# Performance work log

Measured on AMD Instinct MI355X. Metric: run time of the kernel, lower is better.

The kernel has to match this reference:

```python
import jax, jax.numpy as jnp
import numpy as np

DT = 0.01
NJ = 7
GRAV = 9.81
Q_LOWER = jnp.array([-2.9671, -1.8326, -2.9671, -3.1416, -2.9671, -0.0873, -2.9671], jnp.float32)
Q_UPPER = jnp.array([ 2.9671,  1.8326,  2.9671,  0.0,     2.9671,  3.8223,  2.9671], jnp.float32)


def _skew(v):
    z = jnp.zeros((), v.dtype)
    return jnp.stack([jnp.stack([z, -v[2], v[1]]),
                      jnp.stack([v[2], z, -v[0]]),
                      jnp.stack([-v[1], v[0], z])])


def _mot_X(E, r):
    # 6x6 spatial motion transform [[E,0],[-E*skew(r),E]]
    zero = jnp.zeros_like(E)
    top = jnp.concatenate([E, zero], axis=1)
    bot = jnp.concatenate([-E @ _skew(r), E], axis=1)
    return jnp.concatenate([top, bot], axis=0)


def _crm(v):
    # spatial motion cross-product matrix for v=[w;v0]
    Sw, Sv = _skew(v[:3]), _skew(v[3:])
    zero = jnp.zeros_like(Sw)
    top = jnp.concatenate([Sw, zero], axis=1)
    bot = jnp.concatenate([Sv, Sw], axis=1)
    return jnp.concatenate([top, bot], axis=0)


def _step_single(x, u, axes, R_tree, p_tree, I_sp):
    dt_ = x.dtype
    q = jnp.clip(x[:NJ], Q_LOWER.astype(dt_), Q_UPPER.astype(dt_))
    qd = x[NJ:]
    # forward kinematics: per-joint 6x6 child<-parent transforms and motion subspaces
    Xups, Ss = [], []
    eye3 = jnp.eye(3, dtype=dt_)
    for i in range(NJ):
        a = axes[i]
        c, s = jnp.cos(q[i]), jnp.sin(q[i])
        R = c * eye3 + s * _skew(a) + (1.0 - c) * jnp.outer(a, a)  # rodrigues
        Xj = _mot_X(R.T, jnp.zeros(3, dt_))
        Xt = _mot_X(R_tree[i], p_tree[i])
        Xups.append(Xj @ Xt)
        Ss.append(jnp.concatenate([a, jnp.zeros(3, dt_)]))
    # RNEA bias force h (qdd=0, gravity, zero base velocity, identity base pose)
    v_prev = jnp.zeros(6, dt_)
    a_prev = jnp.array([0.0, 0.0, 0.0, 0.0, 0.0, GRAV], dt_)  # a_base = -g trick
    fs = []
    for i in range(NJ):
        vJ = Ss[i] * qd[i]
        v = Xups[i] @ v_prev + vJ
        acc = Xups[i] @ a_prev + _crm(v) @ vJ
        Iv = I_sp[i] @ v
        f = I_sp[i] @ acc - _crm(v).T @ Iv  # crf(v) = -crm(v)^T
        fs.append(f)
        v_prev, a_prev = v, acc
    h = [None] * NJ
    for i in range(NJ - 1, -1, -1):
        h[i] = Ss[i] @ fs[i]
        if i > 0:
            fs[i - 1] = fs[i - 1] + Xups[i].T @ fs[i]
    h = jnp.stack(h)
    # CRBA mass matrix (serial chain, parent(i)=i-1)
    Ic = [I_sp[i] for i in range(NJ)]
    M = jnp.zeros((NJ, NJ), dt_)
    for i in range(NJ - 1, -1, -1):
        if i > 0:
            Ic[i - 1] = Ic[i - 1] + Xups[i].T @ Ic[i] @ Xups[i]
        F = Ic[i] @ Ss[i]
        M = M.at[i, i].set(Ss[i] @ F)
        for j in range(i - 1, -1, -1):
            F = Xups[j + 1].T @ F
            mij = Ss[j] @ F
            M = M.at[i, j].set(mij).at[j, i].set(mij)
    M = M + 1e-8 * jnp.eye(NJ, dtype=dt_)
    qdd = jnp.linalg.solve(M, (u - h)[:, None])[:, 0]
    qd_new = qd + DT * qdd
    q_new = q + DT * qd_new
    return jnp.concatenate([q_new, qd_new])


def setup_inputs() -> dict:
    B = 65536
    key = jax.random.key(0)
    k1, k2 = jax.random.split(key)
    x = jax.random.normal(k1, (B, 14), jnp.float32)
    u = jax.random.normal(k2, (B, 7), jnp.float32)
    rng = np.random.default_rng(0)
    # unit joint axes
    axes = rng.normal(size=(NJ, 3))
    axes = axes / np.linalg.norm(axes, axis=1, keepdims=True)
    # orthonormal fixed parent->child rotations (det +1)
    R_tree = np.empty((NJ, 3, 3))
    for i in range(NJ):
        Q, _ = np.linalg.qr(rng.normal(size=(3, 3)))
        if np.linalg.det(Q) < 0:
            Q[:, 0] = -Q[:, 0]
        R_tree[i] = Q
    p_tree = 0.2 * rng.normal(size=(NJ, 3))
    # SPD 6x6 spatial inertias: [[Ibar, m*Cx],[m*Cx^T, m*I3]]
    I_sp = np.empty((NJ, 6, 6))
    for i in range(NJ):
        m = float(rng.uniform(1.0, 5.0))
        c = 0.05 * rng.normal(size=3)
        Cx = np.array([[0, -c[2], c[1]], [c[2], 0, -c[0]], [-c[1], c[0], 0]])
        A = 0.1 * rng.normal(size=(3, 3))
        Ic_ = A @ A.T + 0.05 * np.eye(3)
        Ibar = Ic_ + m * Cx @ Cx.T
        I_sp[i] = np.block([[Ibar, m * Cx], [m * Cx.T, m * np.eye(3)]])
    return {
        "x": x, "u": u,
        "axes": jnp.asarray(axes, jnp.float32),
        "R_tree": jnp.asarray(R_tree, jnp.float32),
        "p_tree": jnp.asarray(p_tree, jnp.float32),
        "I_sp": jnp.asarray(I_sp, jnp.float32),
    }


def reference(x, u, axes, R_tree, p_tree, I_sp):
    return jax.vmap(_step_single, in_axes=(0, 0, None, None, None, None))(
        x, u, axes, R_tree, p_tree, I_sp)
```

## Files before the change

kernel.cpp:

```cpp
#include <hip/hip_runtime.h>
#include <math.h>

#define NJ 7
#define DTF 0.01f
#define GRAVF 9.81f
#define MIX(i,j) ((i)*((i)+1)/2 + (j))
#define MPAD 29

__device__ __forceinline__ void cross3(const float* a, const float* b, float* o){
    o[0] = a[1]*b[2] - a[2]*b[1];
    o[1] = a[2]*b[0] - a[0]*b[2];
    o[2] = a[0]*b[1] - a[1]*b[0];
}
__device__ __forceinline__ void mv3(const float* E, const float* x, float* y){
    y[0] = E[0]*x[0] + E[1]*x[1] + E[2]*x[2];
    y[1] = E[3]*x[0] + E[4]*x[1] + E[5]*x[2];
    y[2] = E[6]*x[0] + E[7]*x[1] + E[8]*x[2];
}
__device__ __forceinline__ void mtv3(const float* E, const float* x, float* y){
    y[0] = E[0]*x[0] + E[3]*x[1] + E[6]*x[2];
    y[1] = E[1]*x[0] + E[4]*x[1] + E[7]*x[2];
    y[2] = E[2]*x[0] + E[5]*x[1] + E[8]*x[2];
}
__device__ __forceinline__ void mm3(const float* A, const float* B, float* o){
#pragma unroll
    for (int r = 0; r < 3; r++){
#pragma unroll
        for (int c = 0; c < 3; c++){
            o[r*3+c] = A[r*3]*B[c] + A[r*3+1]*B[3+c] + A[r*3+2]*B[6+c];
        }
    }
}
__device__ __forceinline__ void congr(const float* E, const float* X, float* o){
    float t[9];
#pragma unroll
    for (int r = 0; r < 3; r++){
#pragma unroll
        for (int c = 0; c < 3; c++){
            t[r*3+c] = E[r]*X[c] + E[3+r]*X[3+c] + E[6+r]*X[6+c];
        }
    }
    mm3(t, E, o);
}
__device__ __forceinline__ void makeE(const float* a, float s, float c,
                                      const float* Rt, float* Eo){
    float omc = 1.0f - c;
    float RT[9];
    RT[0] = c + omc*a[0]*a[0];       RT[1] =  s*a[2] + omc*a[0]*a[1]; RT[2] = -s*a[1] + omc*a[0]*a[2];
    RT[3] = -s*a[2] + omc*a[1]*a[0]; RT[4] = c + omc*a[1]*a[1];       RT[5] =  s*a[0] + omc*a[1]*a[2];
    RT[6] =  s*a[1] + omc*a[2]*a[0]; RT[7] = -s*a[0] + omc*a[2]*a[1]; RT[8] = c + omc*a[2]*a[2];
    mm3(RT, Rt, Eo);
}

__global__ __launch_bounds__(128)
void panda_step(const float* __restrict__ x, const float* __restrict__ u,
                const float* __restrict__ g_ax, const float* __restrict__ g_Rt,
                const float* __restrict__ g_pt, const float* __restrict__ g_I,
                float* __restrict__ out, int B)
{
    __shared__ float s_ax[NJ*3], s_Rt[NJ*9], s_pt[NJ*3], s_A[NJ*9], s_h[NJ*3], s_m[NJ];
    __shared__ float s_M[64*MPAD];
    if (threadIdx.x < NJ){
        int i = threadIdx.x;
#pragma unroll
        for (int k = 0; k < 3; k++){ s_ax[i*3+k] = g_ax[i*3+k]; s_pt[i*3+k] = g_pt[i*3+k]; }
#pragma unroll
        for (int k = 0; k < 9; k++) s_Rt[i*9+k] = g_Rt[i*9+k];
        const float* I6 = g_I + i*36;
#pragma unroll
        for (int r = 0; r < 3; r++)
#pragma unroll
            for (int c = 0; c < 3; c++) s_A[i*9+r*3+c] = I6[r*6+c];
        s_h[i*3+0] = I6[2*6+3+1];
        s_h[i*3+1] = I6[0*6+3+2];
        s_h[i*3+2] = I6[1*6+3+0];
        s_m[i]     = I6[3*6+3];
    }
    __syncthreads();

    const int role = threadIdx.x >> 6;
    const int lane = threadIdx.x & 63;
    const int e    = blockIdx.x*64 + lane;
    const bool act = (e < B);

    const float QL[NJ] = {-2.9671f,-1.8326f,-2.9671f,-3.1416f,-2.9671f,-0.0873f,-2.9671f};
    const float QU[NJ] = { 2.9671f, 1.8326f, 2.9671f, 0.0f,    2.9671f, 3.8223f, 2.9671f};

    float q[NJ], qd[NJ], sn[NJ], cs[NJ];
    if (act){
        float xl[14];
        const float2* x2 = (const float2*)(x + e*14);
#pragma unroll
        for (int i = 0; i < 7; i++){ float2 v = x2[i]; xl[2*i] = v.x; xl[2*i+1] = v.y; }
#pragma unroll
        for (int i = 0; i < NJ; i++){
            q[i]  = fminf(fmaxf(xl[i], QL[i]), QU[i]);
            qd[i] = xl[NJ + i];
            __sincosf(q[i], &sn[i], &cs[i]);
        }
    }

    float rhs[NJ];

    if (act && role == 1){
        float SA[6], hc[3], mc;
        {
            const float* A6 = &s_A[6*9];
            SA[0]=A6[0]; SA[1]=A6[1]; SA[2]=A6[2]; SA[3]=A6[4]; SA[4]=A6[5]; SA[5]=A6[8];
            hc[0]=s_h[18]; hc[1]=s_h[19]; hc[2]=s_h[20];
            mc = s_m[6];
        }
        float Fk[NJ][6];
        float Mx[28];
#pragma unroll
        for (int i = NJ-1; i >= 0; i--){
            const float* a = &s_ax[i*3];
            const float* p = &s_pt[i*3];
            Fk[i][0] = SA[0]*a[0] + SA[1]*a[1] + SA[2]*a[2];
            Fk[i][1] = SA[1]*a[0] + SA[3]*a[1] + SA[4]*a[2];
            Fk[i][2] = SA[2]*a[0] + SA[4]*a[1] + SA[5]*a[2];
            Fk[i][3] = a[1]*hc[2] - a[2]*hc[1];
            Fk[i][4] = a[2]*hc[0] - a[0]*hc[2];
            Fk[i][5] = a[0]*hc[1] - a[1]*hc[0];
#pragma unroll
            for (int k = i; k < NJ; k++)
                Mx[MIX(k,i)] = a[0]*Fk[k][0] + a[1]*Fk[k][1] + a[2]*Fk[k][2];
            if (i > 0){
                float E[9]; makeE(a, sn[i], cs[i], &s_Rt[i*9], E);
                float Af[9] = {SA[0],SA[1],SA[2], SA[1],SA[3],SA[4], SA[2],SA[4],SA[5]};
                float Ap[9]; congr(E, Af, Ap);
                float hr[3]; mtv3(E, hc, hr);
                float hpd = hr[0]*p[0]+hr[1]*p[1]+hr[2]*p[2];
                float ppd = p[0]*p[0]+p[1]*p[1]+p[2]*p[2];
                float dga = 2.0f*hpd + mc*ppd;
                const float* An = &s_A[(i-1)*9];
                SA[0] = Ap[0] - 2.0f*p[0]*hr[0] - mc*p[0]*p[0] + dga + An[0];
                SA[1] = Ap[1] - p[0]*hr[1] - hr[0]*p[1] - mc*p[0]*p[1] + An[1];
                SA[2] = Ap[2] - p[0]*hr[2] - hr[0]*p[2] - mc*p[0]*p[2] + An[2];
                SA[3] = Ap[4] - 2.0f*p[1]*hr[1] - mc*p[1]*p[1] + dga + An[4];
                SA[4] = Ap[5] - p[1]*hr[2] - hr[1]*p[2] - mc*p[1]*p[2] + An[5];
                SA[5] = Ap[8] - 2.0f*p[2]*hr[2] - mc*p[2]*p[2] + dga + An[8];
                hc[0] = hr[0] + mc*p[0] + s_h[(i-1)*3+0];
                hc[1] = hr[1] + mc*p[1] + s_h[(i-1)*3+1];
                hc[2] = hr[2] + mc*p[2] + s_h[(i-1)*3+2];
                mc += s_m[i-1];
#pragma unroll
                for (int k = i; k < NJ; k++){
                    float tm[3], tf[3], cp[3];
                    mtv3(E, &Fk[k][0], tm); mtv3(E, &Fk[k][3], tf);
                    cross3(p, tf, cp);
                    Fk[k][0]=tm[0]+cp[0]; Fk[k][1]=tm[1]+cp[1]; Fk[k][2]=tm[2]+cp[2];
                    Fk[k][3]=tf[0];       Fk[k][4]=tf[1];       Fk[k][5]=tf[2];
                }
            }
        }
#pragma unroll
        for (int j = 0; j < 28; j++) s_M[lane*MPAD + j] = Mx[j];
    }
    else if (act){
#pragma unroll
        for (int i = 0; i < NJ; i++) rhs[i] = u[e*NJ + i];
        float FF[NJ][6];
        float w[3]  = {0.f,0.f,0.f}, vl[3] = {0.f,0.f,0.f};
        float aw[3] = {0.f,0.f,0.f}, av[3] = {0.f,0.f,GRAVF};
#pragma unroll
        for (int i = 0; i < NJ; i++){
            const float* a = &s_ax[i*3];
            const float* p = &s_pt[i*3];
            float E[9]; makeE(a, sn[i], cs[i], &s_Rt[i*9], E);
            float qdi = qd[i];
            float tw[3]; mv3(E, w, tw);
            float nw[3] = { tw[0]+a[0]*qdi, tw[1]+a[1]*qdi, tw[2]+a[2]*qdi };
            float cwp[3]; cross3(w, p, cwp);
            float t1[3] = { vl[0]+cwp[0], vl[1]+cwp[1], vl[2]+cwp[2] };
            float nvl[3]; mv3(E, t1, nvl);
            float taw[3]; mv3(E, aw, taw);
            float cna[3]; cross3(nw, a, cna);
            float naw[3] = { taw[0]+qdi*cna[0], taw[1]+qdi*cna[1], taw[2]+qdi*cna[2] };
            float cap[3]; cross3(aw, p, cap);
            float t2[3] = { av[0]+cap[0], av[1]+cap[1], av[2]+cap[2] };
            float tav[3]; mv3(E, t2, tav);
            float cva[3]; cross3(nvl, a, cva);
            float nav[3] = { tav[0]+qdi*cva[0], tav[1]+qdi*cva[1], tav[2]+qdi*cva[2] };
            const float* Ai = &s_A[i*9];
            const float* hi = &s_h[i*3];
            float mi = s_m[i];
            float Ivt[3], Iat[3], hxv[3], hxa[3];
            mv3(Ai, nw, Ivt);  cross3(hi, nvl, hxv);
            mv3(Ai, naw, Iat); cross3(hi, nav, hxa);
#pragma unroll
            for (int k = 0; k < 3; k++){ Ivt[k] += hxv[k]; Iat[k] += hxa[k]; }
            float hxw[3], hxaw[3];
            cross3(hi, nw, hxw); cross3(hi, naw, hxaw);
            float Ivb[3] = { mi*nvl[0]-hxw[0], mi*nvl[1]-hxw[1], mi*nvl[2]-hxw[2] };
            float Iab[3] = { mi*nav[0]-hxaw[0], mi*nav[1]-hxaw[1], mi*nav[2]-hxaw[2] };
            float c1[3], c2[3], c3[3];
            cross3(nw, Ivt, c1); cross3(nvl, Ivb, c2); cross3(nw, Ivb, c3);
            FF[i][0] = Iat[0]+c1[0]+c2[0];
            FF[i][1] = Iat[1]+c1[1]+c2[1];
            FF[i][2] = Iat[2]+c1[2]+c2[2];
            FF[i][3] = Iab[0]+c3[0];
            FF[i][4] = Iab[1]+c3[1];
            FF[i][5] = Iab[2]+c3[2];
#pragma unroll
            for (int k = 0; k < 3; k++){ w[k]=nw[k]; vl[k]=nvl[k]; aw[k]=naw[k]; av[k]=nav[k]; }
        }
#pragma unroll
        for (int i = NJ-1; i >= 0; i--){
            const float* a = &s_ax[i*3];
            rhs[i] -= a[0]*FF[i][0] + a[1]*FF[i][1] + a[2]*FF[i][2];
            if (i > 0){
                const float* p = &s_pt[i*3];
                float E[9]; makeE(a, sn[i], cs[i], &s_Rt[i*9], E);
                float tm[3], tf[3], cp[3];
                mtv3(E, &FF[i][0], tm); mtv3(E, &FF[i][3], tf);
                cross3(p, tf, cp);
                FF[i-1][0]+=tm[0]+cp[0]; FF[i-1][1]+=tm[1]+cp[1]; FF[i-1][2]+=tm[2]+cp[2];
                FF[i-1][3]+=tf[0];       FF[i-1][4]+=tf[1];       FF[i-1][5]+=tf[2];
            }
        }
    }

    __syncthreads();

    if (act && role == 0){
        float Mx[28];
#pragma unroll
        for (int j = 0; j < 28; j++) Mx[j] = s_M[lane*MPAD + j];
#pragma unroll
        for (int i = 0; i < NJ; i++) Mx[MIX(i,i)] += 1e-8f;

#pragma unroll
        for (int k = 0; k < NJ; k++){
            float d = Mx[MIX(k,k)];
#pragma unroll
            for (int j = 0; j < NJ; j++) if (j < k) d -= Mx[MIX(k,j)]*Mx[MIX(k,j)];
            float linv = __builtin_amdgcn_rsqf(d);
            Mx[MIX(k,k)] = linv;
#pragma unroll
            for (int i = k+1; i < NJ; i++){
                float s2 = Mx[MIX(i,k)];
#pragma unroll
                for (int j = 0; j < NJ; j++) if (j < k) s2 -= Mx[MIX(i,j)]*Mx[MIX(k,j)];
                Mx[MIX(i,k)] = s2 * linv;
            }
        }
        float y[NJ];
#pragma unroll
        for (int i = 0; i < NJ; i++){
            float s2 = rhs[i];
#pragma unroll
            for (int j = 0; j < NJ; j++) if (j < i) s2 -= Mx[MIX(i,j)]*y[j];
            y[i] = s2 * Mx[MIX(i,i)];
        }
        float z[NJ];
#pragma unroll
        for (int i = NJ-1; i >= 0; i--){
            float s2 = y[i];
#pragma unroll
            for (int j = NJ-1; j >= 0; j--) if (j > i) s2 -= Mx[MIX(j,i)]*z[j];
            z[i] = s2 * Mx[MIX(i,i)];
        }

        float o14[14];
#pragma unroll
        for (int i = 0; i < NJ; i++){
            float qdn = qd[i] + DTF*z[i];
            o14[i]      = q[i] + DTF*qdn;
            o14[NJ + i] = qdn;
        }
        float2* o2 = (float2*)(out + e*14);
#pragma unroll
        for (int i = 0; i < 7; i++){ float2 v; v.x = o14[2*i]; v.y = o14[2*i+1]; o2[i] = v; }
    }
}

extern "C" void kernel_launch(void* const* d_in, const int* in_sizes, int n_in,
                              void* d_out, int out_size, void* d_ws, size_t ws_size,
                              hipStream_t stream) {
    const float* x   = (const float*)d_in[0];
    const float* u   = (const float*)d_in[1];
    const float* ax  = (const float*)d_in[2];
    const float* Rt  = (const float*)d_in[3];
    const float* pt  = (const float*)d_in[4];
    const float* Isp = (const float*)d_in[5];
    float* out = (float*)d_out;
    int B = in_sizes[0] / 14;
    int grid = (B + 63) / 64;
    hipLaunchKernelGGL(panda_step, dim3(grid), dim3(128), 0, stream,
                       x, u, ax, Rt, pt, Isp, out, B);
}
```

Measured before the change: 82.67 us.

## Precompute per-joint rotation basis in prep kernel and read constants from global

Adds a tiny prep kernel that folds the fixed tree rotation into three basis matrices, so each joint rotation E becomes c*B0 - s*B1 + (1-c)*B2 instead of building the Rodrigues matrix and doing a 3x3 matmul. It also packs the axes, offsets and inertia terms into a workspace buffer. The main kernel reads these constants straight from global (uniform, cacheable) memory, which removes the shared-memory staging and the initial block barrier. The cost is a second kernel launch and reliance on scalar or L1 caching of the constant table.

```diff
diff --git a/kernel.cpp b/kernel.cpp
--- a/kernel.cpp
+++ b/kernel.cpp
@@ -6,6 +6,8 @@
 #define GRAVF 9.81f
 #define MIX(i,j) ((i)*((i)+1)/2 + (j))
 #define MPAD 29
+#define CW 44
+
 
 __device__ __forceinline__ void cross3(const float* a, const float* b, float* o){
     o[0] = a[1]*b[2] - a[2]*b[1];
@@ -22,61 +24,66 @@
     y[1] = E[1]*x[0] + E[4]*x[1] + E[7]*x[2];
     y[2] = E[2]*x[0] + E[5]*x[1] + E[8]*x[2];
 }
+__device__ __forceinline__ void symv(const float* S, const float* x, float* y){
+    y[0] = S[0]*x[0] + S[1]*x[1] + S[2]*x[2];
+    y[1] = S[1]*x[0] + S[3]*x[1] + S[4]*x[2];
+    y[2] = S[2]*x[0] + S[4]*x[1] + S[5]*x[2];
+}
 __device__ __forceinline__ void mm3(const float* A, const float* B, float* o){
 #pragma unroll
-    for (int r = 0; r < 3; r++){
-#pragma unroll
-        for (int c = 0; c < 3; c++){
+    for (int r = 0; r < 3; r++)
+#pragma unroll
+        for (int c = 0; c < 3; c++)
             o[r*3+c] = A[r*3]*B[c] + A[r*3+1]*B[3+c] + A[r*3+2]*B[6+c];
-        }
-    }
 }
 __device__ __forceinline__ void congr(const float* E, const float* X, float* o){
     float t[9];
 #pragma unroll
-    for (int r = 0; r < 3; r++){
-#pragma unroll
-        for (int c = 0; c < 3; c++){
+    for (int r = 0; r < 3; r++)
+#pragma unroll
+        for (int c = 0; c < 3; c++)
             t[r*3+c] = E[r]*X[c] + E[3+r]*X[3+c] + E[6+r]*X[6+c];
-        }
-    }
     mm3(t, E, o);
 }
-__device__ __forceinline__ void makeE(const float* a, float s, float c,
-                                      const float* Rt, float* Eo){
+__device__ __forceinline__ void makeE(const float* __restrict__ cb, float s, float c, float* E){
     float omc = 1.0f - c;
-    float RT[9];
-    RT[0] = c + omc*a[0]*a[0];       RT[1] =  s*a[2] + omc*a[0]*a[1]; RT[2] = -s*a[1] + omc*a[0]*a[2];
-    RT[3] = -s*a[2] + omc*a[1]*a[0]; RT[4] = c + omc*a[1]*a[1];       RT[5] =  s*a[0] + omc*a[1]*a[2];
-    RT[6] =  s*a[1] + omc*a[2]*a[0]; RT[7] = -s*a[0] + omc*a[2]*a[1]; RT[8] = c + omc*a[2]*a[2];
-    mm3(RT, Rt, Eo);
+#pragma unroll
+    for (int k = 0; k < 9; k++) E[k] = c*cb[k] - s*cb[9+k] + omc*cb[18+k];
+}
+
+__global__ void panda_prep(const float* __restrict__ g_ax, const float* __restrict__ g_Rt,
+                           const float* __restrict__ g_pt, const float* __restrict__ g_I,
+                           float* __restrict__ cst)
+{
+    int i = threadIdx.x;
+    if (i >= NJ) return;
+    float a0 = g_ax[i*3], a1 = g_ax[i*3+1], a2 = g_ax[i*3+2];
+    const float* R = g_Rt + i*9;
+    float* o = cst + i*CW;
+#pragma unroll
+    for (int k = 0; k < 9; k++) o[k] = R[k];
+#pragma unroll
+    for (int c = 0; c < 3; c++){
+        o[9+c]  = -a2*R[3+c] + a1*R[6+c];
+        o[12+c] =  a2*R[c]   - a0*R[6+c];
+        o[15+c] = -a1*R[c]   + a0*R[3+c];
+        float d =  a0*R[c] + a1*R[3+c] + a2*R[6+c];
+        o[18+c] = a0*d; o[21+c] = a1*d; o[24+c] = a2*d;
+    }
+    o[27]=a0; o[28]=a1; o[29]=a2;
+    o[30]=g_pt[i*3]; o[31]=g_pt[i*3+1]; o[32]=g_pt[i*3+2];
+    const float* I6 = g_I + i*36;
+    o[33]=I6[0];  o[34]=I6[1];  o[35]=I6[2];
+    o[36]=I6[7];  o[37]=I6[8];  o[38]=I6[14];
+    o[39]=I6[16]; o[40]=I6[5];  o[41]=I6[9];
+    o[42]=I6[21];
 }
 
 __global__ __launch_bounds__(128)
 void panda_step(const float* __restrict__ x, const float* __restrict__ u,
-                const float* __restrict__ g_ax, const float* __restrict__ g_Rt,
-                const float* __restrict__ g_pt, const float* __restrict__ g_I,
-                float* __restrict__ out, int B)
+                const float* __restrict__ cst, float* __restrict__ out, int B)
 {
-    __shared__ float s_ax[NJ*3], s_Rt[NJ*9], s_pt[NJ*3], s_A[NJ*9], s_h[NJ*3], s_m[NJ];
     __shared__ float s_M[64*MPAD];
-    if (threadIdx.x < NJ){
-        int i = threadIdx.x;
-#pragma unroll
-        for (int k = 0; k < 3; k++){ s_ax[i*3+k] = g_ax[i*3+k]; s_pt[i*3+k] = g_pt[i*3+k]; }
-#pragma unroll
-        for (int k = 0; k < 9; k++) s_Rt[i*9+k] = g_Rt[i*9+k];
-        const float* I6 = g_I + i*36;
-#pragma unroll
-        for (int r = 0; r < 3; r++)
-#pragma unroll
-            for (int c = 0; c < 3; c++) s_A[i*9+r*3+c] = I6[r*6+c];
-        s_h[i*3+0] = I6[2*6+3+1];
-        s_h[i*3+1] = I6[0*6+3+2];
-        s_h[i*3+2] = I6[1*6+3+0];
-        s_m[i]     = I6[3*6+3];
-    }
-    __syncthreads();
 
     const int role = threadIdx.x >> 6;
     const int lane = threadIdx.x & 63;
@@ -103,22 +110,18 @@
     float rhs[NJ];
 
     if (act && role == 1){
-        float SA[6], hc[3], mc;
-        {
-            const float* A6 = &s_A[6*9];
-            SA[0]=A6[0]; SA[1]=A6[1]; SA[2]=A6[2]; SA[3]=A6[4]; SA[4]=A6[5]; SA[5]=A6[8];
-            hc[0]=s_h[18]; hc[1]=s_h[19]; hc[2]=s_h[20];
-            mc = s_m[6];
-        }
+        const float* cb6 = cst + 6*CW;
+        float SA[6] = {cb6[33],cb6[34],cb6[35],cb6[36],cb6[37],cb6[38]};
+        float hc[3] = {cb6[39],cb6[40],cb6[41]};
+        float mc = cb6[42];
         float Fk[NJ][6];
         float Mx[28];
 #pragma unroll
         for (int i = NJ-1; i >= 0; i--){
-            const float* a = &s_ax[i*3];
-            const float* p = &s_pt[i*3];
-            Fk[i][0] = SA[0]*a[0] + SA[1]*a[1] + SA[2]*a[2];
-            Fk[i][1] = SA[1]*a[0] + SA[3]*a[1] + SA[4]*a[2];
-            Fk[i][2] = SA[2]*a[0] + SA[4]*a[1] + SA[5]*a[2];
+            const float* cb = cst + i*CW;
+            const float* a = cb+27;
+            const float* p = cb+30;
+            symv(SA, a, &Fk[i][0]);
             Fk[i][3] = a[1]*hc[2] - a[2]*hc[1];
             Fk[i][4] = a[2]*hc[0] - a[0]*hc[2];
             Fk[i][5] = a[0]*hc[1] - a[1]*hc[0];
@@ -126,24 +129,24 @@
             for (int k = i; k < NJ; k++)
                 Mx[MIX(k,i)] = a[0]*Fk[k][0] + a[1]*Fk[k][1] + a[2]*Fk[k][2];
             if (i > 0){
-                float E[9]; makeE(a, sn[i], cs[i], &s_Rt[i*9], E);
+                float E[9]; makeE(cb, sn[i], cs[i], E);
                 float Af[9] = {SA[0],SA[1],SA[2], SA[1],SA[3],SA[4], SA[2],SA[4],SA[5]};
                 float Ap[9]; congr(E, Af, Ap);
                 float hr[3]; mtv3(E, hc, hr);
                 float hpd = hr[0]*p[0]+hr[1]*p[1]+hr[2]*p[2];
                 float ppd = p[0]*p[0]+p[1]*p[1]+p[2]*p[2];
                 float dga = 2.0f*hpd + mc*ppd;
-                const float* An = &s_A[(i-1)*9];
-                SA[0] = Ap[0] - 2.0f*p[0]*hr[0] - mc*p[0]*p[0] + dga + An[0];
-                SA[1] = Ap[1] - p[0]*hr[1] - hr[0]*p[1] - mc*p[0]*p[1] + An[1];
-                SA[2] = Ap[2] - p[0]*hr[2] - hr[0]*p[2] - mc*p[0]*p[2] + An[2];
-                SA[3] = Ap[4] - 2.0f*p[1]*hr[1] - mc*p[1]*p[1] + dga + An[4];
-                SA[4] = Ap[5] - p[1]*hr[2] - hr[1]*p[2] - mc*p[1]*p[2] + An[5];
-                SA[5] = Ap[8] - 2.0f*p[2]*hr[2] - mc*p[2]*p[2] + dga + An[8];
-                hc[0] = hr[0] + mc*p[0] + s_h[(i-1)*3+0];
-                hc[1] = hr[1] + mc*p[1] + s_h[(i-1)*3+1];
-                hc[2] = hr[2] + mc*p[2] + s_h[(i-1)*3+2];
-                mc += s_m[i-1];
+                const float* cn = cst + (i-1)*CW;
+                SA[0] = Ap[0] - 2.0f*p[0]*hr[0] - mc*p[0]*p[0] + dga + cn[33];
+                SA[1] = Ap[1] - p[0]*hr[1] - hr[0]*p[1] - mc*p[0]*p[1] + cn[34];
+                SA[2] = Ap[2] - p[0]*hr[2] - hr[0]*p[2] - mc*p[0]*p[2] + cn[35];
+                SA[3] = Ap[4] - 2.0f*p[1]*hr[1] - mc*p[1]*p[1] + dga + cn[36];
+                SA[4] = Ap[5] - p[1]*hr[2] - hr[1]*p[2] - mc*p[1]*p[2] + cn[37];
+                SA[5] = Ap[8] - 2.0f*p[2]*hr[2] - mc*p[2]*p[2] + dga + cn[38];
+                hc[0] = hr[0] + mc*p[0] + cn[39];
+                hc[1] = hr[1] + mc*p[1] + cn[40];
+                hc[2] = hr[2] + mc*p[2] + cn[41];
+                mc += cn[42];
 #pragma unroll
                 for (int k = i; k < NJ; k++){
                     float tm[3], tf[3], cp[3];
@@ -165,9 +168,10 @@
         float aw[3] = {0.f,0.f,0.f}, av[3] = {0.f,0.f,GRAVF};
 #pragma unroll
         for (int i = 0; i < NJ; i++){
-            const float* a = &s_ax[i*3];
-            const float* p = &s_pt[i*3];
-            float E[9]; makeE(a, sn[i], cs[i], &s_Rt[i*9], E);
+            const float* cb = cst + i*CW;
+            const float* a = cb+27;
+            const float* p = cb+30;
+            float E[9]; makeE(cb, sn[i], cs[i], E);
             float qdi = qd[i];
             float tw[3]; mv3(E, w, tw);
             float nw[3] = { tw[0]+a[0]*qdi, tw[1]+a[1]*qdi, tw[2]+a[2]*qdi };
@@ -182,12 +186,12 @@
             float tav[3]; mv3(E, t2, tav);
             float cva[3]; cross3(nvl, a, cva);
             float nav[3] = { tav[0]+qdi*cva[0], tav[1]+qdi*cva[1], tav[2]+qdi*cva[2] };
-            const float* Ai = &s_A[i*9];
-            const float* hi = &s_h[i*3];
-            float mi = s_m[i];
+            const float* SAi = cb+33;
+            const float* hi  = cb+39;
+            float mi = cb[42];
             float Ivt[3], Iat[3], hxv[3], hxa[3];
-            mv3(Ai, nw, Ivt);  cross3(hi, nvl, hxv);
-            mv3(Ai, naw, Iat); cross3(hi, nav, hxa);
+            symv(SAi, nw, Ivt);  cross3(hi, nvl, hxv);
+            symv(SAi, naw, Iat); cross3(hi, nav, hxa);
 #pragma unroll
             for (int k = 0; k < 3; k++){ Ivt[k] += hxv[k]; Iat[k] += hxa[k]; }
             float hxw[3], hxaw[3];
@@ -207,11 +211,12 @@
         }
 #pragma unroll
         for (int i = NJ-1; i >= 0; i--){
-            const float* a = &s_ax[i*3];
+            const float* cb = cst + i*CW;
+            const float* a = cb+27;
             rhs[i] -= a[0]*FF[i][0] + a[1]*FF[i][1] + a[2]*FF[i][2];
             if (i > 0){
-                const float* p = &s_pt[i*3];
-                float E[9]; makeE(a, sn[i], cs[i], &s_Rt[i*9], E);
+                const float* p = cb+30;
+                float E[9]; makeE(cb, sn[i], cs[i], E);
                 float tm[3], tf[3], cp[3];
                 mtv3(E, &FF[i][0], tm); mtv3(E, &FF[i][3], tf);
                 cross3(p, tf, cp);
@@ -285,8 +290,10 @@
     const float* pt  = (const float*)d_in[4];
     const float* Isp = (const float*)d_in[5];
     float* out = (float*)d_out;
+    float* cst = (float*)d_ws;
     int B = in_sizes[0] / 14;
+    hipLaunchKernelGGL(panda_prep, dim3(1), dim3(64), 0, stream, ax, Rt, pt, Isp, cst);
     int grid = (B + 63) / 64;
     hipLaunchKernelGGL(panda_step, dim3(grid), dim3(128), 0, stream,
-                       x, u, ax, Rt, pt, Isp, out, B);
-}
+                       x, u, cst, out, B);
+}
```

Result: no change. 82.87 us (+0.2%).

## Recast RNEA and CRBA in base-frame coordinates and move Cholesky to mass-matrix warp

Applied to the files above, without the earlier changes.

Both the mass-matrix and bias-force paths now compute cumulative base-frame rotations and joint axes once. Dynamics are expressed in base coordinates, so the backward passes become plain prefix sums instead of repeated 6x6 transform applications. The Cholesky factorisation moves from the solve warp to the mass-matrix warp to balance work between the two roles. Shared-memory staging of the constant model parameters is dropped in favour of direct global/constant loads, which removes a block-wide sync but may raise register pressure.

```diff
diff --git a/kernel.cpp b/kernel.cpp
--- a/kernel.cpp
+++ b/kernel.cpp
@@ -12,45 +12,74 @@
     o[1] = a[2]*b[0] - a[0]*b[2];
     o[2] = a[0]*b[1] - a[1]*b[0];
 }
-__device__ __forceinline__ void mv3(const float* E, const float* x, float* y){
-    y[0] = E[0]*x[0] + E[1]*x[1] + E[2]*x[2];
-    y[1] = E[3]*x[0] + E[4]*x[1] + E[5]*x[2];
-    y[2] = E[6]*x[0] + E[7]*x[1] + E[8]*x[2];
-}
 __device__ __forceinline__ void mtv3(const float* E, const float* x, float* y){
     y[0] = E[0]*x[0] + E[3]*x[1] + E[6]*x[2];
     y[1] = E[1]*x[0] + E[4]*x[1] + E[7]*x[2];
     y[2] = E[2]*x[0] + E[5]*x[1] + E[8]*x[2];
 }
+__device__ __forceinline__ void symv(const float* S, const float* x, float* y){
+    y[0] = S[0]*x[0] + S[1]*x[1] + S[2]*x[2];
+    y[1] = S[1]*x[0] + S[3]*x[1] + S[4]*x[2];
+    y[2] = S[2]*x[0] + S[4]*x[1] + S[5]*x[2];
+}
 __device__ __forceinline__ void mm3(const float* A, const float* B, float* o){
 #pragma unroll
-    for (int r = 0; r < 3; r++){
-#pragma unroll
-        for (int c = 0; c < 3; c++){
+    for (int r = 0; r < 3; r++)
+#pragma unroll
+        for (int c = 0; c < 3; c++)
             o[r*3+c] = A[r*3]*B[c] + A[r*3+1]*B[3+c] + A[r*3+2]*B[6+c];
-        }
-    }
 }
 __device__ __forceinline__ void congr(const float* E, const float* X, float* o){
     float t[9];
 #pragma unroll
-    for (int r = 0; r < 3; r++){
-#pragma unroll
-        for (int c = 0; c < 3; c++){
+    for (int r = 0; r < 3; r++)
+#pragma unroll
+        for (int c = 0; c < 3; c++)
             t[r*3+c] = E[r]*X[c] + E[3+r]*X[3+c] + E[6+r]*X[6+c];
-        }
-    }
     mm3(t, E, o);
 }
-__device__ __forceinline__ void makeE(const float* a, float s, float c,
-                                      const float* Rt, float* Eo){
+__device__ __forceinline__ void makeE(const float* a, const float* __restrict__ Rt,
+                                      float s, float c, float* E){
     float omc = 1.0f - c;
     float RT[9];
     RT[0] = c + omc*a[0]*a[0];       RT[1] =  s*a[2] + omc*a[0]*a[1]; RT[2] = -s*a[1] + omc*a[0]*a[2];
     RT[3] = -s*a[2] + omc*a[1]*a[0]; RT[4] = c + omc*a[1]*a[1];       RT[5] =  s*a[0] + omc*a[1]*a[2];
     RT[6] =  s*a[1] + omc*a[2]*a[0]; RT[7] = -s*a[0] + omc*a[2]*a[1]; RT[8] = c + omc*a[2]*a[2];
-    mm3(RT, Rt, Eo);
-}
+    float Rl[9];
+#pragma unroll
+    for (int k = 0; k < 9; k++) Rl[k] = Rt[k];
+    mm3(RT, Rl, E);
+}
+__device__ __forceinline__ void bodyI(const float* __restrict__ g_I, int i,
+                                      float* SA, float* h, float& m){
+    const float* I6 = g_I + i*36;
+    SA[0]=I6[0]; SA[1]=I6[1]; SA[2]=I6[2];
+    SA[3]=I6[7]; SA[4]=I6[8]; SA[5]=I6[14];
+    h[0]=I6[16]; h[1]=I6[5]; h[2]=I6[9];
+    m = I6[21];
+}
+__device__ __forceinline__ void congrBase(const float* Ec, const float* rc,
+                                          const float* SA, const float* h, float m,
+                                          float* SA0, float* h0){
+    float Af[9] = {SA[0],SA[1],SA[2], SA[1],SA[3],SA[4], SA[2],SA[4],SA[5]};
+    float Ap[9]; congr(Ec, Af, Ap);
+    float hr[3]; mtv3(Ec, h, hr);
+    float hpd = hr[0]*rc[0]+hr[1]*rc[1]+hr[2]*rc[2];
+    float ppd = rc[0]*rc[0]+rc[1]*rc[1]+rc[2]*rc[2];
+    float dga = 2.0f*hpd + m*ppd;
+    SA0[0] = Ap[0] - 2.0f*rc[0]*hr[0] - m*rc[0]*rc[0] + dga;
+    SA0[1] = Ap[1] - rc[0]*hr[1] - hr[0]*rc[1] - m*rc[0]*rc[1];
+    SA0[2] = Ap[2] - rc[0]*hr[2] - hr[0]*rc[2] - m*rc[0]*rc[2];
+    SA0[3] = Ap[4] - 2.0f*rc[1]*hr[1] - m*rc[1]*rc[1] + dga;
+    SA0[4] = Ap[5] - rc[1]*hr[2] - hr[1]*rc[2] - m*rc[1]*rc[2];
+    SA0[5] = Ap[8] - 2.0f*rc[2]*hr[2] - m*rc[2]*rc[2] + dga;
+    h0[0] = hr[0] + m*rc[0];
+    h0[1] = hr[1] + m*rc[1];
+    h0[2] = hr[2] + m*rc[2];
+}
+
+__constant__ float QL_c[NJ] = {-2.9671f,-1.8326f,-2.9671f,-3.1416f,-2.9671f,-0.0873f,-2.9671f};
+__constant__ float QU_c[NJ] = { 2.9671f, 1.8326f, 2.9671f, 0.0f,    2.9671f, 3.8223f, 2.9671f};
 
 __global__ __launch_bounds__(128)
 void panda_step(const float* __restrict__ x, const float* __restrict__ u,
@@ -58,34 +87,13 @@
                 const float* __restrict__ g_pt, const float* __restrict__ g_I,
                 float* __restrict__ out, int B)
 {
-    __shared__ float s_ax[NJ*3], s_Rt[NJ*9], s_pt[NJ*3], s_A[NJ*9], s_h[NJ*3], s_m[NJ];
     __shared__ float s_M[64*MPAD];
-    if (threadIdx.x < NJ){
-        int i = threadIdx.x;
-#pragma unroll
-        for (int k = 0; k < 3; k++){ s_ax[i*3+k] = g_ax[i*3+k]; s_pt[i*3+k] = g_pt[i*3+k]; }
-#pragma unroll
-        for (int k = 0; k < 9; k++) s_Rt[i*9+k] = g_Rt[i*9+k];
-        const float* I6 = g_I + i*36;
-#pragma unroll
-        for (int r = 0; r < 3; r++)
-#pragma unroll
-            for (int c = 0; c < 3; c++) s_A[i*9+r*3+c] = I6[r*6+c];
-        s_h[i*3+0] = I6[2*6+3+1];
-        s_h[i*3+1] = I6[0*6+3+2];
-        s_h[i*3+2] = I6[1*6+3+0];
-        s_m[i]     = I6[3*6+3];
-    }
-    __syncthreads();
 
     const int role = threadIdx.x >> 6;
     const int lane = threadIdx.x & 63;
     const int e    = blockIdx.x*64 + lane;
     const bool act = (e < B);
 
-    const float QL[NJ] = {-2.9671f,-1.8326f,-2.9671f,-3.1416f,-2.9671f,-0.0873f,-2.9671f};
-    const float QU[NJ] = { 2.9671f, 1.8326f, 2.9671f, 0.0f,    2.9671f, 3.8223f, 2.9671f};
-
     float q[NJ], qd[NJ], sn[NJ], cs[NJ];
     if (act){
         float xl[14];
@@ -94,7 +102,7 @@
         for (int i = 0; i < 7; i++){ float2 v = x2[i]; xl[2*i] = v.x; xl[2*i+1] = v.y; }
 #pragma unroll
         for (int i = 0; i < NJ; i++){
-            q[i]  = fminf(fmaxf(xl[i], QL[i]), QU[i]);
+            q[i]  = fminf(fmaxf(xl[i], QL_c[i]), QU_c[i]);
             qd[i] = xl[NJ + i];
             __sincosf(q[i], &sn[i], &cs[i]);
         }
@@ -103,55 +111,70 @@
     float rhs[NJ];
 
     if (act && role == 1){
-        float SA[6], hc[3], mc;
-        {
-            const float* A6 = &s_A[6*9];
-            SA[0]=A6[0]; SA[1]=A6[1]; SA[2]=A6[2]; SA[3]=A6[4]; SA[4]=A6[5]; SA[5]=A6[8];
-            hc[0]=s_h[18]; hc[1]=s_h[19]; hc[2]=s_h[20];
-            mc = s_m[6];
-        }
-        float Fk[NJ][6];
+        float Sw[NJ][3], Sv[NJ][3];
+        float SB[NJ][6], hB[NJ][3];
+        float Ec[9], rc[3];
+#pragma unroll
+        for (int i = 0; i < NJ; i++){
+            float a[3] = { g_ax[3*i], g_ax[3*i+1], g_ax[3*i+2] };
+            float p[3] = { g_pt[3*i], g_pt[3*i+1], g_pt[3*i+2] };
+            float E[9]; makeE(a, g_Rt + 9*i, sn[i], cs[i], E);
+            if (i == 0){
+#pragma unroll
+                for (int k = 0; k < 9; k++) Ec[k] = E[k];
+                rc[0]=p[0]; rc[1]=p[1]; rc[2]=p[2];
+            } else {
+                float t3[3]; mtv3(Ec, p, t3);
+                rc[0]+=t3[0]; rc[1]+=t3[1]; rc[2]+=t3[2];
+                float En[9]; mm3(E, Ec, En);
+#pragma unroll
+                for (int k = 0; k < 9; k++) Ec[k] = En[k];
+            }
+            float sh[3]; mtv3(Ec, a, sh);
+            float cb[3]; cross3(rc, sh, cb);
+#pragma unroll
+            for (int k = 0; k < 3; k++){ Sw[i][k]=sh[k]; Sv[i][k]=cb[k]; }
+            float SAb[6], hb[3], mb; bodyI(g_I, i, SAb, hb, mb);
+            congrBase(Ec, rc, SAb, hb, mb, &SB[i][0], &hB[i][0]);
+        }
+        float IcA[6] = {0,0,0,0,0,0}, Ich[3] = {0,0,0}, Icm = 0.f;
         float Mx[28];
 #pragma unroll
         for (int i = NJ-1; i >= 0; i--){
-            const float* a = &s_ax[i*3];
-            const float* p = &s_pt[i*3];
-            Fk[i][0] = SA[0]*a[0] + SA[1]*a[1] + SA[2]*a[2];
-            Fk[i][1] = SA[1]*a[0] + SA[3]*a[1] + SA[4]*a[2];
-            Fk[i][2] = SA[2]*a[0] + SA[4]*a[1] + SA[5]*a[2];
-            Fk[i][3] = a[1]*hc[2] - a[2]*hc[1];
-            Fk[i][4] = a[2]*hc[0] - a[0]*hc[2];
-            Fk[i][5] = a[0]*hc[1] - a[1]*hc[0];
-#pragma unroll
-            for (int k = i; k < NJ; k++)
-                Mx[MIX(k,i)] = a[0]*Fk[k][0] + a[1]*Fk[k][1] + a[2]*Fk[k][2];
-            if (i > 0){
-                float E[9]; makeE(a, sn[i], cs[i], &s_Rt[i*9], E);
-                float Af[9] = {SA[0],SA[1],SA[2], SA[1],SA[3],SA[4], SA[2],SA[4],SA[5]};
-                float Ap[9]; congr(E, Af, Ap);
-                float hr[3]; mtv3(E, hc, hr);
-                float hpd = hr[0]*p[0]+hr[1]*p[1]+hr[2]*p[2];
-                float ppd = p[0]*p[0]+p[1]*p[1]+p[2]*p[2];
-                float dga = 2.0f*hpd + mc*ppd;
-                const float* An = &s_A[(i-1)*9];
-                SA[0] = Ap[0] - 2.0f*p[0]*hr[0] - mc*p[0]*p[0] + dga + An[0];
-                SA[1] = Ap[1] - p[0]*hr[1] - hr[0]*p[1] - mc*p[0]*p[1] + An[1];
-                SA[2] = Ap[2] - p[0]*hr[2] - hr[0]*p[2] - mc*p[0]*p[2] + An[2];
-                SA[3] = Ap[4] - 2.0f*p[1]*hr[1] - mc*p[1]*p[1] + dga + An[4];
-                SA[4] = Ap[5] - p[1]*hr[2] - hr[1]*p[2] - mc*p[1]*p[2] + An[5];
-                SA[5] = Ap[8] - 2.0f*p[2]*hr[2] - mc*p[2]*p[2] + dga + An[8];
-                hc[0] = hr[0] + mc*p[0] + s_h[(i-1)*3+0];
-                hc[1] = hr[1] + mc*p[1] + s_h[(i-1)*3+1];
-                hc[2] = hr[2] + mc*p[2] + s_h[(i-1)*3+2];
-                mc += s_m[i-1];
-#pragma unroll
-                for (int k = i; k < NJ; k++){
-                    float tm[3], tf[3], cp[3];
-                    mtv3(E, &Fk[k][0], tm); mtv3(E, &Fk[k][3], tf);
-                    cross3(p, tf, cp);
-                    Fk[k][0]=tm[0]+cp[0]; Fk[k][1]=tm[1]+cp[1]; Fk[k][2]=tm[2]+cp[2];
-                    Fk[k][3]=tf[0];       Fk[k][4]=tf[1];       Fk[k][5]=tf[2];
-                }
+#pragma unroll
+            for (int k = 0; k < 6; k++) IcA[k] += SB[i][k];
+#pragma unroll
+            for (int k = 0; k < 3; k++) Ich[k] += hB[i][k];
+            Icm += g_I[i*36 + 21];
+            float Ft[3], Fb[3], t1[3], t2[3];
+            symv(IcA, &Sw[i][0], Ft);
+            cross3(Ich, &Sv[i][0], t1);
+#pragma unroll
+            for (int k = 0; k < 3; k++) Ft[k] += t1[k];
+            cross3(Ich, &Sw[i][0], t2);
+#pragma unroll
+            for (int k = 0; k < 3; k++) Fb[k] = Icm*Sv[i][k] - t2[k];
+#pragma unroll
+            for (int j = 0; j < NJ; j++) if (j <= i){
+                Mx[MIX(i,j)] = Sw[j][0]*Ft[0] + Sw[j][1]*Ft[1] + Sw[j][2]*Ft[2]
+                             + Sv[j][0]*Fb[0] + Sv[j][1]*Fb[1] + Sv[j][2]*Fb[2];
+            }
+        }
+#pragma unroll
+        for (int i = 0; i < NJ; i++) Mx[MIX(i,i)] += 1e-8f;
+#pragma unroll
+        for (int k = 0; k < NJ; k++){
+            float d = Mx[MIX(k,k)];
+#pragma unroll
+            for (int j = 0; j < NJ; j++) if (j < k) d -= Mx[MIX(k,j)]*Mx[MIX(k,j)];
+            float linv = __builtin_amdgcn_rsqf(d);
+            Mx[MIX(k,k)] = linv;
+#pragma unroll
+            for (int i2 = k+1; i2 < NJ; i2++){
+                float s2 = Mx[MIX(i2,k)];
+#pragma unroll
+                for (int j = 0; j < NJ; j++) if (j < k) s2 -= Mx[MIX(i2,j)]*Mx[MIX(k,j)];
+                Mx[MIX(i2,k)] = s2 * linv;
             }
         }
 #pragma unroll
@@ -160,64 +183,68 @@
     else if (act){
 #pragma unroll
         for (int i = 0; i < NJ; i++) rhs[i] = u[e*NJ + i];
-        float FF[NJ][6];
-        float w[3]  = {0.f,0.f,0.f}, vl[3] = {0.f,0.f,0.f};
-        float aw[3] = {0.f,0.f,0.f}, av[3] = {0.f,0.f,GRAVF};
-#pragma unroll
-        for (int i = 0; i < NJ; i++){
-            const float* a = &s_ax[i*3];
-            const float* p = &s_pt[i*3];
-            float E[9]; makeE(a, sn[i], cs[i], &s_Rt[i*9], E);
+        float Sw[NJ][3], Sv[NJ][3];
+        float f0[NJ][6];
+        float Ec[9], rc[3];
+        float vw[3]={0,0,0}, vv[3]={0,0,0};
+        float aw[3]={0,0,0}, av[3]={0,0,GRAVF};
+#pragma unroll
+        for (int i = 0; i < NJ; i++){
+            float a[3] = { g_ax[3*i], g_ax[3*i+1], g_ax[3*i+2] };
+            float p[3] = { g_pt[3*i], g_pt[3*i+1], g_pt[3*i+2] };
+            float E[9]; makeE(a, g_Rt + 9*i, sn[i], cs[i], E);
+            if (i == 0){
+#pragma unroll
+                for (int k = 0; k < 9; k++) Ec[k] = E[k];
+                rc[0]=p[0]; rc[1]=p[1]; rc[2]=p[2];
+            } else {
+                float t3[3]; mtv3(Ec, p, t3);
+                rc[0]+=t3[0]; rc[1]+=t3[1]; rc[2]+=t3[2];
+                float En[9]; mm3(E, Ec, En);
+#pragma unroll
+                for (int k = 0; k < 9; k++) Ec[k] = En[k];
+            }
+            float sh[3]; mtv3(Ec, a, sh);
+            float cb[3]; cross3(rc, sh, cb);
+#pragma unroll
+            for (int k = 0; k < 3; k++){ Sw[i][k]=sh[k]; Sv[i][k]=cb[k]; }
             float qdi = qd[i];
-            float tw[3]; mv3(E, w, tw);
-            float nw[3] = { tw[0]+a[0]*qdi, tw[1]+a[1]*qdi, tw[2]+a[2]*qdi };
-            float cwp[3]; cross3(w, p, cwp);
-            float t1[3] = { vl[0]+cwp[0], vl[1]+cwp[1], vl[2]+cwp[2] };
-            float nvl[3]; mv3(E, t1, nvl);
-            float taw[3]; mv3(E, aw, taw);
-            float cna[3]; cross3(nw, a, cna);
-            float naw[3] = { taw[0]+qdi*cna[0], taw[1]+qdi*cna[1], taw[2]+qdi*cna[2] };
-            float cap[3]; cross3(aw, p, cap);
-            float t2[3] = { av[0]+cap[0], av[1]+cap[1], av[2]+cap[2] };
-            float tav[3]; mv3(E, t2, tav);
-            float cva[3]; cross3(nvl, a, cva);
-            float nav[3] = { tav[0]+qdi*cva[0], tav[1]+qdi*cva[1], tav[2]+qdi*cva[2] };
-            const float* Ai = &s_A[i*9];
-            const float* hi = &s_h[i*3];
-            float mi = s_m[i];
-            float Ivt[3], Iat[3], hxv[3], hxa[3];
-            mv3(Ai, nw, Ivt);  cross3(hi, nvl, hxv);
-            mv3(Ai, naw, Iat); cross3(hi, nav, hxa);
-#pragma unroll
-            for (int k = 0; k < 3; k++){ Ivt[k] += hxv[k]; Iat[k] += hxa[k]; }
-            float hxw[3], hxaw[3];
-            cross3(hi, nw, hxw); cross3(hi, naw, hxaw);
-            float Ivb[3] = { mi*nvl[0]-hxw[0], mi*nvl[1]-hxw[1], mi*nvl[2]-hxw[2] };
-            float Iab[3] = { mi*nav[0]-hxaw[0], mi*nav[1]-hxaw[1], mi*nav[2]-hxaw[2] };
+#pragma unroll
+            for (int k = 0; k < 3; k++){ vw[k] += qdi*sh[k]; vv[k] += qdi*cb[k]; }
             float c1[3], c2[3], c3[3];
-            cross3(nw, Ivt, c1); cross3(nvl, Ivb, c2); cross3(nw, Ivb, c3);
-            FF[i][0] = Iat[0]+c1[0]+c2[0];
-            FF[i][1] = Iat[1]+c1[1]+c2[1];
-            FF[i][2] = Iat[2]+c1[2]+c2[2];
-            FF[i][3] = Iab[0]+c3[0];
-            FF[i][4] = Iab[1]+c3[1];
-            FF[i][5] = Iab[2]+c3[2];
-#pragma unroll
-            for (int k = 0; k < 3; k++){ w[k]=nw[k]; vl[k]=nvl[k]; aw[k]=naw[k]; av[k]=nav[k]; }
-        }
+            cross3(vw, sh, c1); cross3(vw, cb, c2); cross3(vv, sh, c3);
+#pragma unroll
+            for (int k = 0; k < 3; k++){ aw[k] += qdi*c1[k]; av[k] += qdi*(c2[k]+c3[k]); }
+            float SAb[6], hb[3], mb; bodyI(g_I, i, SAb, hb, mb);
+            float SA0[6], h0[3]; congrBase(Ec, rc, SAb, hb, mb, SA0, h0);
+            float Ivt[3], Ivb[3], Iat[3], Iab[3], t1[3], t2[3];
+            symv(SA0, vw, Ivt); cross3(h0, vv, t1);
+#pragma unroll
+            for (int k = 0; k < 3; k++) Ivt[k] += t1[k];
+            cross3(h0, vw, t2);
+#pragma unroll
+            for (int k = 0; k < 3; k++) Ivb[k] = mb*vv[k] - t2[k];
+            symv(SA0, aw, Iat); cross3(h0, av, t1);
+#pragma unroll
+            for (int k = 0; k < 3; k++) Iat[k] += t1[k];
+            cross3(h0, aw, t2);
+#pragma unroll
+            for (int k = 0; k < 3; k++) Iab[k] = mb*av[k] - t2[k];
+            float d1[3], d2[3], d3[3];
+            cross3(vw, Ivt, d1); cross3(vv, Ivb, d2); cross3(vw, Ivb, d3);
+#pragma unroll
+            for (int k = 0; k < 3; k++){
+                f0[i][k]   = Iat[k] + d1[k] + d2[k];
+                f0[i][3+k] = Iab[k] + d3[k];
+            }
+        }
+        float g6[6] = {0,0,0,0,0,0};
 #pragma unroll
         for (int i = NJ-1; i >= 0; i--){
-            const float* a = &s_ax[i*3];
-            rhs[i] -= a[0]*FF[i][0] + a[1]*FF[i][1] + a[2]*FF[i][2];
-            if (i > 0){
-                const float* p = &s_pt[i*3];
-                float E[9]; makeE(a, sn[i], cs[i], &s_Rt[i*9], E);
-                float tm[3], tf[3], cp[3];
-                mtv3(E, &FF[i][0], tm); mtv3(E, &FF[i][3], tf);
-                cross3(p, tf, cp);
-                FF[i-1][0]+=tm[0]+cp[0]; FF[i-1][1]+=tm[1]+cp[1]; FF[i-1][2]+=tm[2]+cp[2];
-                FF[i-1][3]+=tf[0];       FF[i-1][4]+=tf[1];       FF[i-1][5]+=tf[2];
-            }
+#pragma unroll
+            for (int k = 0; k < 6; k++) g6[k] += f0[i][k];
+            rhs[i] -= Sw[i][0]*g6[0] + Sw[i][1]*g6[1] + Sw[i][2]*g6[2]
+                    + Sv[i][0]*g6[3] + Sv[i][1]*g6[4] + Sv[i][2]*g6[5];
         }
     }
 
@@ -227,24 +254,6 @@
         float Mx[28];
 #pragma unroll
         for (int j = 0; j < 28; j++) Mx[j] = s_M[lane*MPAD + j];
-#pragma unroll
-        for (int i = 0; i < NJ; i++) Mx[MIX(i,i)] += 1e-8f;
-
-#pragma unroll
-        for (int k = 0; k < NJ; k++){
-            float d = Mx[MIX(k,k)];
-#pragma unroll
-            for (int j = 0; j < NJ; j++) if (j < k) d -= Mx[MIX(k,j)]*Mx[MIX(k,j)];
-            float linv = __builtin_amdgcn_rsqf(d);
-            Mx[MIX(k,k)] = linv;
-#pragma unroll
-            for (int i = k+1; i < NJ; i++){
-                float s2 = Mx[MIX(i,k)];
-#pragma unroll
-                for (int j = 0; j < NJ; j++) if (j < k) s2 -= Mx[MIX(i,j)]*Mx[MIX(k,j)];
-                Mx[MIX(i,k)] = s2 * linv;
-            }
-        }
         float y[NJ];
 #pragma unroll
         for (int i = 0; i < NJ; i++){
@@ -261,7 +270,6 @@
             for (int j = NJ-1; j >= 0; j--) if (j > i) s2 -= Mx[MIX(j,i)]*z[j];
             z[i] = s2 * Mx[MIX(i,i)];
         }
-
         float o14[14];
 #pragma unroll
         for (int i = 0; i < NJ; i++){
```

Result: no change. 83.84 us (+1.4%).
